# Optimization experiments

Hardware: AMD Instinct MI355X
Metric: run time of the kernel (lower is better)

## Reference

```python
import jax, jax.numpy as jnp
import numpy as np

B, C, R, E, H = 32, 64, 63, 256, 4
D = E // H  # head dim = 64


def setup_inputs() -> dict:
    key = jax.random.key(0)
    ks = jax.random.split(key, 8)
    s = 0.02
    return {
        "x": jax.random.normal(ks[0], (B, C, R, E), jnp.float32),
        "real_cols": jax.random.randint(ks[1], (B,), 0, C),
        "cls_token": jax.random.normal(ks[2], (E,), jnp.float32),
        "w_in": (jax.random.normal(ks[3], (3 * E, E), jnp.float32) * s),
        "b_in": jnp.zeros((3 * E,), jnp.float32),
        "w_out": (jax.random.normal(ks[4], (E, E), jnp.float32) * s),
        "b_out": jnp.zeros((E,), jnp.float32),
        "ln_g": jnp.ones((E,), jnp.float32),
        "ln_b": jnp.zeros((E,), jnp.float32),
        "w1": (jax.random.normal(ks[5], (E, E), jnp.float32) * s),
        "b1": jnp.zeros((E,), jnp.float32),
        "w2": (jax.random.normal(ks[6], (E, E), jnp.float32) * s),
        "b2": jnp.zeros((E,), jnp.float32),
    }


def reference(x, real_cols, cls_token, w_in, b_in, w_out, b_out, ln_g, ln_b, w1, b1, w2, b2):
    # x: (B, C, R, E); one fused batched MHA+LN+FFN over all (B, C) columns.
    Bq, Cq, Rq, Eq = x.shape
    S = Rq + 1
    cls = jnp.broadcast_to(cls_token, (Bq, Cq, 1, Eq))
    seq = jnp.concatenate([cls, x], axis=2)  # (B,C,S,E)

    # torch MultiheadAttention in-projection: x @ W^T + b, packed q|k|v
    qkv = seq @ w_in.T + b_in  # (B,C,S,3E)
    q, k, v = jnp.split(qkv, 3, axis=-1)
    q = q.reshape(Bq, Cq, S, H, D)
    k = k.reshape(Bq, Cq, S, H, D)
    v = v.reshape(Bq, Cq, S, H, D)

    scale = 1.0 / jnp.sqrt(jnp.asarray(D, x.dtype))
    scores = jnp.einsum('bcqhd,bckhd->bchqk', q, k) * scale  # (B,C,H,S,S)
    attn = jax.nn.softmax(scores, axis=-1)
    ctx = jnp.einsum('bchqk,bckhd->bcqhd', attn, v).reshape(Bq, Cq, S, Eq)
    attn_out = ctx @ w_out.T + b_out  # (B,C,S,E)

    # LayerNorm (biased variance, eps=1e-5 as in torch)
    mu = attn_out.mean(axis=-1, keepdims=True)
    var = ((attn_out - mu) ** 2).mean(axis=-1, keepdims=True)
    ln = (attn_out - mu) / jnp.sqrt(var + 1e-5) * ln_g + ln_b

    ffn = jax.nn.relu(ln @ w1.T + b1) @ w2.T + b2
    out = ln + ffn  # (B,C,S,E)

    rep = out[:, :, 0, :]  # rep_mode == 'cls'

    # columns >= real_cols[b] are zero-padded, matching the original loop
    mask = jnp.arange(Cq)[None, :] < real_cols[:, None]
    return jnp.where(mask[..., None], rep, jnp.zeros((), x.dtype))
```

## Files before the change

kernel.cpp:

```cpp
#include <hip/hip_runtime.h>
#include <hip/hip_bf16.h>
#include <cstdint>

typedef unsigned short u16;
typedef uint32_t u32;

#define Bq 32
#define Cq 64
#define Rq 63
#define NB 4
#define SEQ_ST 264

typedef __attribute__((ext_vector_type(8))) short bf16x8;
typedef __attribute__((ext_vector_type(4))) float f32x4;

__device__ __forceinline__ float bflo(u32 u){ return __uint_as_float(u << 16); }
__device__ __forceinline__ float bfhi(u32 u){ return __uint_as_float(u & 0xffff0000u); }
__device__ __forceinline__ float bf1(u16 u){ return __uint_as_float(((u32)u) << 16); }
__device__ __forceinline__ u16 tobf(float f){ __hip_bfloat16 h = __float2bfloat16(f); return *(u16*)&h; }

__device__ __forceinline__ bool dtype_is_bf16(const void* ln_g){
    return *(const u32*)ln_g == 0x3F803F80u;
}
__device__ __forceinline__ float ldin(const void* p, int i, bool bf){
    return bf ? bf1(((const u16*)p)[i]) : ((const float*)p)[i];
}


__global__ __launch_bounds__(256) void prep_kernel(
    const void* __restrict__ cls, const void* __restrict__ w_in,
    const void* __restrict__ b_in, const void* __restrict__ w_out,
    const void* __restrict__ w1, const void* __restrict__ w2,
    const void* __restrict__ ln_g_flag,
    u16* __restrict__ uB,
    u16* __restrict__ wvT, u16* __restrict__ woT,
    u16* __restrict__ w1T, u16* __restrict__ w2T)
{
    const bool bf = dtype_is_bf16(ln_g_flag);
    const int tid = threadIdx.x;
    const int blk = blockIdx.x;
    __shared__ float q0[256];
    __shared__ __align__(16) float clsf[256];

    if (blk < 256) {
        const int e = blk, j = tid;
        const int dsti = (((e >> 4) * 512) + ((j >> 5) * 64) + (((j >> 3) & 3) * 16) + (e & 15)) * 8 + (j & 7);
        wvT[dsti] = tobf(ldin(w_in, (512 + e) * 256 + j, bf));
        woT[dsti] = tobf(ldin(w_out, e * 256 + j, bf));
        w1T[dsti] = tobf(ldin(w1,    e * 256 + j, bf));
        w2T[dsti] = tobf(ldin(w2,    e * 256 + j, bf));
        return;
    }

    const int h = blk - 256;
    clsf[tid] = ldin(cls, tid, bf);
    __syncthreads();

    {
        float acc = ldin(b_in, tid, bf);
        if (bf) {
            const u16* wr = (const u16*)w_in + tid * 256;
            #pragma unroll 8
            for (int j8 = 0; j8 < 32; ++j8) {
                uint4 w = *(const uint4*)(wr + j8 * 8);
                const float* c = &clsf[j8 * 8];
                acc += bflo(w.x) * c[0] + bfhi(w.x) * c[1]
                     + bflo(w.y) * c[2] + bfhi(w.y) * c[3]
                     + bflo(w.z) * c[4] + bfhi(w.z) * c[5]
                     + bflo(w.w) * c[6] + bfhi(w.w) * c[7];
            }
        } else {
            const float4* wr = (const float4*)((const float*)w_in + tid * 256);
            #pragma unroll 8
            for (int j4 = 0; j4 < 64; ++j4) {
                float4 w = wr[j4];
                float4 c = *(const float4*)&clsf[j4 * 4];
                acc += w.x * c.x + w.y * c.y + w.z * c.z + w.w * c.w;
            }
        }
        q0[tid] = acc;
    }
    __syncthreads();

    {
        float ua = 0.f;
        const int j = tid;
        #pragma unroll 8
        for (int d = 0; d < 64; ++d)
            ua += q0[h * 64 + d] * ldin(w_in, (256 + h * 64 + d) * 256 + j, bf);
        const int base = ((j >> 5) * 64) + (((j >> 3) & 3) * 16);
        const int ii = j & 7;
        uB[(base + h)      * 8 + ii] = tobf(ua * 0.125f);
        uB[(base + h + 4)  * 8 + ii] = 0;
        uB[(base + h + 8)  * 8 + ii] = 0;
        uB[(base + h + 12) * 8 + ii] = 0;
    }
}

__device__ __forceinline__ void mfma_layer4(const u16* __restrict__ wbase,
                                            const u16* __restrict__ Abase,
                                            int lane, int w,
                                            f32x4 acc[4])
{
    bf16x8 af[8];
    const u16* ap = Abase + (lane & 15) * SEQ_ST + (lane >> 4) * 8;
    #pragma unroll
    for (int ks = 0; ks < 8; ++ks)
        af[ks] = *(const bf16x8*)(ap + ks * 32);
    const u16* wp0 = wbase + (((w * 4) * 512 + lane) << 3);
    #pragma unroll
    for (int ks = 0; ks < 8; ++ks) {
        #pragma unroll
        for (int nt = 0; nt < 4; ++nt) {
            bf16x8 bfr = *(const bf16x8*)(wp0 + ((nt * 512 + ks * 64) << 3));
            acc[nt] = __builtin_amdgcn_mfma_f32_16x16x32_bf16(af[ks], bfr, acc[nt], 0, 0, 0);
        }
    }
}

__global__ __launch_bounds__(256) void fused_kernel(
    const void* __restrict__ x, const int* __restrict__ real_cols,
    const void* __restrict__ cls,
    const void* __restrict__ b_in, const void* __restrict__ b_out,
    const void* __restrict__ ln_g, const void* __restrict__ ln_b,
    const void* __restrict__ b1p, const void* __restrict__ b2p,
    const u16* __restrict__ uBg,
    const u16* __restrict__ wvT, const u16* __restrict__ woT,
    const u16* __restrict__ w1T, const u16* __restrict__ w2T,
    void* __restrict__ out)
{
    const bool bf = dtype_is_bf16(ln_g);
    const int tid = threadIdx.x;
    const int b = blockIdx.x >> 4;
    const int g = blockIdx.x & 15;
    const int c0 = g * NB;
    const int rc = real_cols[b];
    const int e = tid;

    if (c0 >= rc) {
        #pragma unroll
        for (int i = 0; i < NB; ++i) {
            size_t oi = (((size_t)b << 6) + c0 + i) * 256 + e;
            if (bf) ((u16*)out)[oi] = 0; else ((float*)out)[oi] = 0.f;
        }
        return;
    }

    __shared__ __align__(16) char smem[58048];
    u16*   seq    = (u16*)smem;
    u16*   ctxB   = (u16*)smem;
    float* aoF    = (float*)(smem + 8448);
    u16*   lnB    = (u16*)(smem + 12544);
    u16*   h1B    = (u16*)(smem + 20992);
    u16*   uB     = (u16*)(smem + 33792);
    float* lds_a  = (float*)(smem + 41984);
    u16*   sB     = (u16*)(smem + 43008);
    float* redA   = (float*)(smem + 57792);
    float* redB   = (float*)(smem + 57856);
    float* redPm  = (float*)(smem + 57920);
    float* redPs  = (float*)(smem + 57984);

    ((uint4*)uB)[tid]       = ((const uint4*)uBg)[tid];
    ((uint4*)uB)[tid + 256] = ((const uint4*)uBg)[tid + 256];

    if (bf) {
        if (tid < 32) {
            uint4 val = *(const uint4*)((const u16*)cls + tid * 8);
            *(uint4*)&seq[tid * 8] = val;
        }
    } else {
        if (tid < 64) {
            float4 v = *(const float4*)((const float*)cls + tid * 4);
            u32 lo = ((u32)tobf(v.y) << 16) | tobf(v.x);
            u32 hi = ((u32)tobf(v.w) << 16) | tobf(v.z);
            *(uint2*)&seq[tid * 4] = make_uint2(lo, hi);
        }
    }

    const int w = tid >> 6, lane = tid & 63;

    uint4 stg[8];
    float4 stgf[16];
    auto load_col = [&](int c) {
        int bc2 = (b << 6) + c;
        if (bf) {
            const u16* xr = (const u16*)x + (size_t)bc2 * (Rq * 256);
            #pragma unroll
            for (int k = 0; k < 8; ++k) {
                int idx = k * 256 + tid;
                if (idx < 2016) stg[k] = *(const uint4*)(xr + idx * 8);
            }
        } else {
            const float* xr = (const float*)x + (size_t)bc2 * (Rq * 256);
            #pragma unroll
            for (int k = 0; k < 16; ++k) {
                int idx = k * 256 + tid;
                if (idx < 4032) stgf[k] = *(const float4*)(xr + idx * 4);
            }
        }
    };
    auto write_col = [&]() {
        if (bf) {
            #pragma unroll
            for (int k = 0; k < 8; ++k) {
                int idx = k * 256 + tid;
                if (idx < 2016) {
                    int tt = (idx >> 5) + 1, col = (idx & 31) * 8;
                    *(uint4*)&seq[tt * SEQ_ST + col] = stg[k];
                }
            }
        } else {
            #pragma unroll
            for (int k = 0; k < 16; ++k) {
                int idx = k * 256 + tid;
                if (idx < 4032) {
                    float4 v = stgf[k];
                    int tt = (idx >> 6) + 1, col = (idx & 63) * 4;
                    u32 lo = ((u32)tobf(v.y) << 16) | tobf(v.x);
                    u32 hi = ((u32)tobf(v.w) << 16) | tobf(v.z);
                    *(uint2*)&seq[tt * SEQ_ST + col] = make_uint2(lo, hi);
                }
            }
        }
    };

    load_col(c0);

    for (int i = 0; i < NB; ++i) {
        const int c = c0 + i;
        const bool act = (c < rc);

        if (act) write_col();
        __syncthreads();

        if (i + 1 < NB && c0 + i + 1 < rc) load_col(c0 + i + 1);

        float mw, ev0, ev1, ev2, ev3;
        if (act) {
            const u16* ap = &seq[(w * 16 + (lane & 15)) * SEQ_ST + (lane >> 4) * 8];
            f32x4 cacc = (f32x4){0.f, 0.f, 0.f, 0.f};
            #pragma unroll
            for (int ks = 0; ks < 8; ++ks) {
                bf16x8 a  = *(const bf16x8*)(ap + ks * 32);
                bf16x8 bb = *(const bf16x8*)(uB + ((ks * 64 + lane) << 3));
                cacc = __builtin_amdgcn_mfma_f32_16x16x32_bf16(a, bb, cacc, 0, 0, 0);
            }
            mw = fmaxf(fmaxf(cacc[0], cacc[1]), fmaxf(cacc[2], cacc[3]));
            mw = fmaxf(mw, __shfl_xor(mw, 16));
            mw = fmaxf(mw, __shfl_xor(mw, 32));
            ev0 = __expf(cacc[0] - mw); ev1 = __expf(cacc[1] - mw);
            ev2 = __expf(cacc[2] - mw); ev3 = __expf(cacc[3] - mw);
            float sw = ev0 + ev1 + ev2 + ev3;
            sw += __shfl_xor(sw, 16);
            sw += __shfl_xor(sw, 32);
            if (lane < 4) { redPm[w * 4 + lane] = mw; redPs[w * 4 + lane] = sw; }
        }
        __syncthreads();

        if (act) {
            const int h2 = lane & 15;
            if (h2 < 4) {
                float m0 = redPm[h2],     m1 = redPm[4 + h2];
                float m2 = redPm[8 + h2], m3 = redPm[12 + h2];
                float M = fmaxf(fmaxf(m0, m1), fmaxf(m2, m3));
                float S = redPs[h2]      * __expf(m0 - M)
                        + redPs[4 + h2]  * __expf(m1 - M)
                        + redPs[8 + h2]  * __expf(m2 - M)
                        + redPs[12 + h2] * __expf(m3 - M);
                float corr = __expf(mw - M) / S;
                int t0 = (w * 16 + (lane >> 4) * 4) * 4 + h2;
                lds_a[t0]      = ev0 * corr;
                lds_a[t0 + 4]  = ev1 * corr;
                lds_a[t0 + 8]  = ev2 * corr;
                lds_a[t0 + 12] = ev3 * corr;
            }
        }
        __syncthreads();

        if (act) {
            float s0 = 0.f, s1 = 0.f, s2 = 0.f, s3 = 0.f;
            #pragma unroll 4
            for (int tt = 0; tt < 64; ++tt) {
                float v = bf1(seq[tt * SEQ_ST + tid]);
                float4 at = *(const float4*)&lds_a[tt * 4];
                s0 += at.x * v; s1 += at.y * v; s2 += at.z * v; s3 += at.w * v;
            }
            sB[(0  + i) * SEQ_ST + tid] = tobf(s0);
            sB[(4  + i) * SEQ_ST + tid] = tobf(s1);
            sB[(8  + i) * SEQ_ST + tid] = tobf(s2);
            sB[(12 + i) * SEQ_ST + tid] = tobf(s3);
        } else {
            sB[(0  + i) * SEQ_ST + tid] = 0;
            sB[(4  + i) * SEQ_ST + tid] = 0;
            sB[(8  + i) * SEQ_ST + tid] = 0;
            sB[(12 + i) * SEQ_ST + tid] = 0;
        }
        __syncthreads();
    }

    f32x4 acc[4];

    #pragma unroll
    for (int nt = 0; nt < 4; ++nt) {
        float bv = ldin(b_in, 512 + w * 64 + nt * 16 + (lane & 15), bf);
        acc[nt] = (f32x4){bv, bv, bv, bv};
    }
    mfma_layer4(wvT, sB + w * 4 * SEQ_ST, lane, w, acc);
    if (lane < 16) {
        #pragma unroll
        for (int nt = 0; nt < 4; ++nt) {
            int n = w * 64 + nt * 16 + lane;
            #pragma unroll
            for (int r = 0; r < 4; ++r) ctxB[r * SEQ_ST + n] = tobf(acc[nt][r]);
        }
    }
    __syncthreads();

    #pragma unroll
    for (int nt = 0; nt < 4; ++nt) {
        float bv = ldin(b_out, w * 64 + nt * 16 + (lane & 15), bf);
        acc[nt] = (f32x4){bv, bv, bv, bv};
    }
    mfma_layer4(woT, ctxB, lane, w, acc);
    if (lane < 16) {
        #pragma unroll
        for (int nt = 0; nt < 4; ++nt) {
            int n = w * 64 + nt * 16 + lane;
            #pragma unroll
            for (int r = 0; r < 4; ++r) aoF[r * 256 + n] = acc[nt][r];
        }
    }
    __syncthreads();

    float ao[NB];
    #pragma unroll
    for (int i = 0; i < NB; ++i) ao[i] = aoF[i * 256 + e];

    float mu[NB];
    {
        float r[NB];
        #pragma unroll
        for (int i = 0; i < NB; ++i) r[i] = ao[i];
        #pragma unroll
        for (int off = 32; off; off >>= 1) {
            #pragma unroll
            for (int i = 0; i < NB; ++i) r[i] += __shfl_xor(r[i], off);
        }
        if (lane == 0) {
            #pragma unroll
            for (int i = 0; i < NB; ++i) redA[w * NB + i] = r[i];
        }
    }
    __syncthreads();
    #pragma unroll
    for (int i = 0; i < NB; ++i)
        mu[i] = (redA[i] + redA[NB + i] + redA[2 * NB + i] + redA[3 * NB + i]) * (1.f / 256.f);

    float lnv[NB];
    {
        float r[NB];
        #pragma unroll
        for (int i = 0; i < NB; ++i) { float d = ao[i] - mu[i]; r[i] = d * d; }
        #pragma unroll
        for (int off = 32; off; off >>= 1) {
            #pragma unroll
            for (int i = 0; i < NB; ++i) r[i] += __shfl_xor(r[i], off);
        }
        if (lane == 0) {
            #pragma unroll
            for (int i = 0; i < NB; ++i) redB[w * NB + i] = r[i];
        }
    }
    __syncthreads();
    {
        float gg = ldin(ln_g, e, bf), bb = ldin(ln_b, e, bf);
        #pragma unroll
        for (int i = 0; i < NB; ++i) {
            float var = (redB[i] + redB[NB + i] + redB[2 * NB + i] + redB[3 * NB + i]) * (1.f / 256.f);
            lnv[i] = (ao[i] - mu[i]) * rsqrtf(var + 1e-5f) * gg + bb;
            lnB[i * SEQ_ST + e] = tobf(lnv[i]);
        }
    }
    __syncthreads();

    #pragma unroll
    for (int nt = 0; nt < 4; ++nt) {
        float bv = ldin(b1p, w * 64 + nt * 16 + (lane & 15), bf);
        acc[nt] = (f32x4){bv, bv, bv, bv};
    }
    mfma_layer4(w1T, lnB, lane, w, acc);
    if (lane < 16) {
        #pragma unroll
        for (int nt = 0; nt < 4; ++nt) {
            int n = w * 64 + nt * 16 + lane;
            #pragma unroll
            for (int r = 0; r < 4; ++r) h1B[r * SEQ_ST + n] = tobf(fmaxf(acc[nt][r], 0.f));
        }
    }
    __syncthreads();

    #pragma unroll
    for (int nt = 0; nt < 4; ++nt) {
        float bv = ldin(b2p, w * 64 + nt * 16 + (lane & 15), bf);
        acc[nt] = (f32x4){bv, bv, bv, bv};
    }
    mfma_layer4(w2T, h1B, lane, w, acc);
    float* oF = aoF;
    if (lane < 16) {
        #pragma unroll
        for (int nt = 0; nt < 4; ++nt) {
            int n = w * 64 + nt * 16 + lane;
            #pragma unroll
            for (int r = 0; r < 4; ++r) oF[r * 256 + n] = acc[nt][r];
        }
    }
    __syncthreads();

    #pragma unroll
    for (int i = 0; i < NB; ++i) {
        int c = c0 + i;
        float val = (c < rc) ? (oF[i * 256 + e] + lnv[i]) : 0.f;
        size_t oi = (((size_t)b << 6) + c) * 256 + e;
        if (bf) ((u16*)out)[oi] = tobf(val); else ((float*)out)[oi] = val;
    }
}

extern "C" void kernel_launch(void* const* d_in, const int* in_sizes, int n_in,
                              void* d_out, int out_size, void* d_ws, size_t ws_size,
                              hipStream_t stream) {
    const void* x     = d_in[0];
    const int* rcols  = (const int*)d_in[1];
    const void* cls   = d_in[2];
    const void* w_in  = d_in[3];
    const void* b_in  = d_in[4];
    const void* w_out = d_in[5];
    const void* b_out = d_in[6];
    const void* ln_g  = d_in[7];
    const void* ln_b  = d_in[8];
    const void* w1    = d_in[9];
    const void* b1    = d_in[10];
    const void* w2    = d_in[11];
    const void* b2    = d_in[12];

    char* ws = (char*)d_ws;
    u16* uB  = (u16*)(ws);
    u16* wvT = (u16*)(ws + 8192);
    u16* woT = (u16*)(ws + 8192 + 131072);
    u16* w1T = (u16*)(ws + 8192 + 2 * 131072);
    u16* w2T = (u16*)(ws + 8192 + 3 * 131072);

    prep_kernel<<<260, 256, 0, stream>>>(cls, w_in, b_in, w_out, w1, w2, ln_g,
                                         uB, wvT, woT, w1T, w2T);
    fused_kernel<<<Bq * (Cq / NB), 256, 0, stream>>>(x, rcols, cls,
                                                     b_in, b_out, ln_g, ln_b,
                                                     b1, b2, uB,
                                                     wvT, woT, w1T, w2T, d_out);
}
```

Measured before the change: 240.0 us.

## Halve columns per block and vectorize attention-weighted sum with bf16 weights

Each block now handles two columns instead of four, which doubles the block count and makes the skipping of padded columns finer-grained. The attention-weighted sum over sequence rows is reorganized so each wave owns one head and each lane four contiguous features. The softmax weights are stored transposed as packed bf16 and read with 16-byte loads, and the sequence values are read with 8-byte loads. This cuts scalar LDS traffic and per-thread loop overhead, at the cost of rounding the attention weights to bf16 and repeating the weight-staging work across more blocks.

```diff
diff --git a/kernel.cpp b/kernel.cpp
--- a/kernel.cpp
+++ b/kernel.cpp
@@ -8,8 +8,9 @@
 #define Bq 32
 #define Cq 64
 #define Rq 63
-#define NB 4
+#define NB 2
 #define SEQ_ST 264
+#define AT_ST 80
 
 typedef __attribute__((ext_vector_type(8))) short bf16x8;
 typedef __attribute__((ext_vector_type(4))) float f32x4;
@@ -131,8 +132,8 @@
 {
     const bool bf = dtype_is_bf16(ln_g);
     const int tid = threadIdx.x;
-    const int b = blockIdx.x >> 4;
-    const int g = blockIdx.x & 15;
+    const int b = blockIdx.x / (Cq / NB);
+    const int g = blockIdx.x % (Cq / NB);
     const int c0 = g * NB;
     const int rc = real_cols[b];
     const int e = tid;
@@ -153,7 +154,7 @@
     u16*   lnB    = (u16*)(smem + 12544);
     u16*   h1B    = (u16*)(smem + 20992);
     u16*   uB     = (u16*)(smem + 33792);
-    float* lds_a  = (float*)(smem + 41984);
+    u16*   aT     = (u16*)(smem + 41984);
     u16*   sB     = (u16*)(smem + 43008);
     float* redA   = (float*)(smem + 57792);
     float* redB   = (float*)(smem + 57856);
@@ -268,32 +269,39 @@
                         + redPs[8 + h2]  * __expf(m2 - M)
                         + redPs[12 + h2] * __expf(m3 - M);
                 float corr = __expf(mw - M) / S;
-                int t0 = (w * 16 + (lane >> 4) * 4) * 4 + h2;
-                lds_a[t0]      = ev0 * corr;
-                lds_a[t0 + 4]  = ev1 * corr;
-                lds_a[t0 + 8]  = ev2 * corr;
-                lds_a[t0 + 12] = ev3 * corr;
+                int t0 = w * 16 + (lane >> 4) * 4;
+                u32 lo = (u32)tobf(ev0 * corr) | ((u32)tobf(ev1 * corr) << 16);
+                u32 hi = (u32)tobf(ev2 * corr) | ((u32)tobf(ev3 * corr) << 16);
+                *(uint2*)&aT[h2 * AT_ST + t0] = make_uint2(lo, hi);
             }
         }
         __syncthreads();
 
-        if (act) {
+        {
+            const int j0 = lane * 4;
             float s0 = 0.f, s1 = 0.f, s2 = 0.f, s3 = 0.f;
-            #pragma unroll 4
-            for (int tt = 0; tt < 64; ++tt) {
-                float v = bf1(seq[tt * SEQ_ST + tid]);
-                float4 at = *(const float4*)&lds_a[tt * 4];
-                s0 += at.x * v; s1 += at.y * v; s2 += at.z * v; s3 += at.w * v;
-            }
-            sB[(0  + i) * SEQ_ST + tid] = tobf(s0);
-            sB[(4  + i) * SEQ_ST + tid] = tobf(s1);
-            sB[(8  + i) * SEQ_ST + tid] = tobf(s2);
-            sB[(12 + i) * SEQ_ST + tid] = tobf(s3);
-        } else {
-            sB[(0  + i) * SEQ_ST + tid] = 0;
-            sB[(4  + i) * SEQ_ST + tid] = 0;
-            sB[(8  + i) * SEQ_ST + tid] = 0;
-            sB[(12 + i) * SEQ_ST + tid] = 0;
+            if (act) {
+                #pragma unroll
+                for (int t0 = 0; t0 < 64; t0 += 8) {
+                    uint4 aq = *(const uint4*)&aT[w * AT_ST + t0];
+                    float aa0 = bflo(aq.x), aa1 = bfhi(aq.x);
+                    float aa2 = bflo(aq.y), aa3 = bfhi(aq.y);
+                    float aa4 = bflo(aq.z), aa5 = bfhi(aq.z);
+                    float aa6 = bflo(aq.w), aa7 = bfhi(aq.w);
+                    const u16* sr = &seq[t0 * SEQ_ST + j0];
+                    #pragma unroll
+                    for (int dt = 0; dt < 8; ++dt) {
+                        uint2 sv = *(const uint2*)(sr + dt * SEQ_ST);
+                        float at = dt == 0 ? aa0 : dt == 1 ? aa1 : dt == 2 ? aa2 : dt == 3 ? aa3
+                                 : dt == 4 ? aa4 : dt == 5 ? aa5 : dt == 6 ? aa6 : aa7;
+                        s0 += at * bflo(sv.x); s1 += at * bfhi(sv.x);
+                        s2 += at * bflo(sv.y); s3 += at * bfhi(sv.y);
+                    }
+                }
+            }
+            u32 lo = (u32)tobf(s0) | ((u32)tobf(s1) << 16);
+            u32 hi = (u32)tobf(s2) | ((u32)tobf(s3) << 16);
+            *(uint2*)&sB[(4 * w + i) * SEQ_ST + j0] = make_uint2(lo, hi);
         }
         __syncthreads();
     }
```

Measured after the change: 263.2 us. +9.7%, slower.
